# Kernel optimization log

Hardware: AMD Instinct MI355X
Metric: run time of the kernel (lower is better)

## Reference

```python
import jax, jax.numpy as jnp
import numpy as np

W0, W1 = 8, 8           # attn_grid_window_size
HEADS = 8
ATTN_CH = 256
HD = ATTN_CH // HEADS   # 32
LN_EPS = 1e-5
L2_EPS = 1e-12


def _rel_pos_index(h, w):
    # Swin-style relative position index, [h*w, h*w] int
    coords = np.stack(np.meshgrid(np.arange(h), np.arange(w), indexing='ij'))  # [2,h,w]
    coords = coords.reshape(2, -1)                                             # [2,L]
    rel = coords[:, :, None] - coords[:, None, :]                              # [2,L,L]
    rel = rel.transpose(1, 2, 0).astype(np.int64)                              # [L,L,2]
    rel[:, :, 0] += h - 1
    rel[:, :, 1] += w - 1
    rel[:, :, 0] *= 2 * w - 1
    return rel.sum(-1)                                                         # [L,L]

_REL_IDX = _rel_pos_index(W0, W1)


def _layernorm2d(x, g, b):
    # nn.LayerNorm((8,8)): normalize over the last two dims, affine shape (8,8)
    mu = jnp.mean(x, axis=(-2, -1), keepdims=True)
    var = jnp.var(x, axis=(-2, -1), keepdims=True)
    return (x - mu) * jax.lax.rsqrt(var + LN_EPS) * g + b


def setup_inputs() -> dict:
    key = jax.random.key(0)
    ks = jax.random.split(key, 8)
    C = 256
    return {
        'X': jax.random.normal(ks[0], (8, C, 128, 128), jnp.float32),
        'pre_gamma': jnp.ones((W0, W1), jnp.float32),
        'pre_beta': jnp.zeros((W0, W1), jnp.float32),
        'post_gamma': jnp.ones((W0, W1), jnp.float32),
        'post_beta': jnp.zeros((W0, W1), jnp.float32),
        'Wqkv': jax.random.normal(ks[1], (3 * ATTN_CH, C), jnp.float32) * 0.02,
        'bqkv': jnp.zeros((3 * ATTN_CH,), jnp.float32),
        'Wproj': jax.random.normal(ks[2], (C, ATTN_CH), jnp.float32) * 0.02,
        'bproj': jnp.zeros((C,), jnp.float32),
        'rel_bias_table': jax.random.normal(ks[3], ((2 * W0 - 1) * (2 * W1 - 1), HEADS), jnp.float32) * 0.02,
    }


def reference(X, pre_gamma, pre_beta, post_gamma, post_beta,
              Wqkv, bqkv, Wproj, bproj, rel_bias_table):
    N, C, H, W = X.shape
    L = W0 * W1
    # --- block partition (mirrors torch view/permute/contiguous().view) ---
    xp = X.reshape(N, C, H // W0, W0, W // W1, W1)
    xp = xp.transpose(0, 2, 4, 3, 5, 1).reshape(-1, C, W0, W1)  # [Bw, C, 8, 8]
    Bw = xp.shape[0]
    # --- pre-norm over the window dims ---
    xn = _layernorm2d(xp, pre_gamma, pre_beta)
    # --- windowed multi-head self-attention with relative position bias ---
    x = xn.reshape(Bw, C, L)
    qkv = jnp.einsum('oc,bcl->bol', Wqkv, x) + bqkv[None, :, None]   # [Bw, 3A, L]
    qkv = qkv.reshape(Bw, 3, HEADS, HD, L)
    q = qkv[:, 0].transpose(0, 1, 3, 2)  # [Bw, h, L, d]
    k = qkv[:, 1].transpose(0, 1, 3, 2)
    v = qkv[:, 2].transpose(0, 1, 3, 2)
    # MetNet-3 qk normalization (L2 normalize instead of 1/sqrt(d) scale)
    q = q / jnp.clip(jnp.linalg.norm(q, axis=-1, keepdims=True), L2_EPS)
    k = k / jnp.clip(jnp.linalg.norm(k, axis=-1, keepdims=True), L2_EPS)
    bias = rel_bias_table[jnp.asarray(_REL_IDX)].transpose(2, 0, 1)  # [h, L, L]
    attn = jnp.einsum('bhld,bhmd->bhlm', q, k) + bias[None]          # [Bw, h, L, L]
    attn = jax.nn.softmax(attn, axis=-1)
    out = jnp.einsum('bhlm,bhmd->bhld', attn, v)                     # [Bw, h, L, d]
    out = out.transpose(0, 1, 3, 2).reshape(Bw, ATTN_CH, L)          # [Bw, A, L]
    out = jnp.einsum('ca,bal->bcl', Wproj, out) + bproj[None, :, None]
    out = out.reshape(Bw, C, W0, W1)
    # --- residual, post-norm + Identity MLP residual ---
    y = xp + out
    y = y + _layernorm2d(y, post_gamma, post_beta)
    # --- reverse partition: composition of torch .view()s == plain reshape ---
    return y.reshape(N, C, H, W)
```

## Files before the change

### kernel.cpp

```cpp
#include <hip/hip_runtime.h>

typedef __bf16 bf16x8 __attribute__((ext_vector_type(8)));
typedef float  f32x4  __attribute__((ext_vector_type(4)));
typedef unsigned short ushort4v __attribute__((ext_vector_type(4)));

#define DEVI static __device__ __forceinline__

#define LDS_FENCE() do { \
  asm volatile("s_waitcnt lgkmcnt(0)" ::: "memory"); \
  __builtin_amdgcn_sched_barrier(0); \
} while (0)

DEVI unsigned short f2bf(float f) {
  __bf16 h = (__bf16)f;
  return __builtin_bit_cast(unsigned short, h);
}
DEVI float bf2f(unsigned short s) {
  union { unsigned u; float f; } v; v.u = ((unsigned)s) << 16;
  return v.f;
}

__global__ void prep_kernel(const float* __restrict__ Wqkv, const float* __restrict__ Wproj,
                            const float* __restrict__ table,
                            unsigned short* __restrict__ wq, unsigned short* __restrict__ wp,
                            float* __restrict__ biasg, float* __restrict__ rowsum) {
  const int i = blockIdx.x * 256 + threadIdx.x;
  if (i < 768 * 256) wq[i] = f2bf(Wqkv[i]);
  if (i < 256 * 256) wp[i] = f2bf(Wproj[i]);
  if (i < 8 * 64 * 64) {
    const int h = i >> 12, r = (i >> 6) & 63, c = i & 63;
    const int ridx = ((r >> 3) - (c >> 3) + 7) * 15 + ((r & 7) - (c & 7) + 7);
    biasg[i] = table[ridx * 8 + h];
  }
  if (i < 768) {
    const float4* p = reinterpret_cast<const float4*>(Wqkv + (size_t)i * 256);
    float s = 0.f;
#pragma unroll
    for (int j = 0; j < 64; ++j) { const float4 a = p[j]; s += a.x + a.y + a.z + a.w; }
    rowsum[i] = s;
  }
}

#define LDS_XN 0u
#define LDS_ST 32768u
#define LDS_Q  34816u
#define LDS_K  75776u
#define LDS_V  116736u
#define LDS_XW 34816u
#define LDS_YO 75776u
#define LDS_TOTAL 149504u

__global__ void __launch_bounds__(512, 2)
win_attn_kernel(const float* __restrict__ X,
                const float* __restrict__ preg, const float* __restrict__ preb,
                const float* __restrict__ postg, const float* __restrict__ postb,
                const float* __restrict__ bqkv, const float* __restrict__ bproj,
                const unsigned short* __restrict__ wq, const unsigned short* __restrict__ wp,
                const float* __restrict__ biasg, const float* __restrict__ rowsum,
                float* __restrict__ out) {
  __shared__ alignas(16) unsigned char sh[LDS_TOTAL];
  const int tid = threadIdx.x;
  const int w = tid >> 6;
  const int lane = tid & 63, lm = lane & 15, lg = lane >> 4;
  const int orig = blockIdx.x;
  const int b = (orig & 7) * 256 + (orig >> 3);
  const int n = b >> 8, gh = (b >> 4) & 15, gw = b & 15;
  const size_t wbase = (size_t)n * 4194304 + (size_t)gh * 1024 + (size_t)gw * 8;

  {
#pragma unroll
    for (int i = 0; i < 4; ++i) {
      const int rid = i * 512 + tid;
      const int cc = rid >> 3, w0 = rid & 7;
      const float* xb = X + wbase + (size_t)cc * 16384 + w0 * 128;
      const float4 a  = *reinterpret_cast<const float4*>(xb);
      const float4 bv = *reinterpret_cast<const float4*>(xb + 4);
      const unsigned xorv = (cc & 64) ? 16u : 0u;
      unsigned char* dst = sh + LDS_XW + (unsigned)cc * 272u + (unsigned)w0 * 32u;
      *reinterpret_cast<float4*>(dst + xorv)         = a;
      *reinterpret_cast<float4*>(dst + (16u ^ xorv)) = bv;
    }
  }
  __syncthreads();

  {
    const int c = tid >> 1, half = tid & 1;
    const int r = ((c >> 5) << 3) + ((c >> 2) & 7);
    const unsigned base = LDS_XW + (unsigned)(c & 3) * (64u * 272u)
                        + 4u * (unsigned)(r ^ ((c & 1) << 2));
    float fv[32];
    float s1 = 0.f, s2 = 0.f;
#pragma unroll
    for (int i = 0; i < 32; ++i) {
      const int l = half * 32 + i;
      const float v = *reinterpret_cast<const float*>(sh + base + (unsigned)l * 272u);
      fv[i] = v; s1 += v; s2 += v * v;
    }
    s1 += __shfl_xor(s1, 1);
    s2 += __shfl_xor(s2, 1);
    const float mean = s1 * (1.f / 64.f);
    float var = s2 * (1.f / 64.f) - mean * mean;
    var = fmaxf(var, 0.f) + 1e-5f;
    const float rstd = rsqrtf(var);
    const float sig  = var * rstd;
#pragma unroll
    for (int i = 0; i < 32; ++i) {
      const int l = half * 32 + i;
      *(unsigned short*)(sh + LDS_XN + l * 512 +
          (((unsigned)(2 * c)) ^ ((unsigned)((l & 7) << 4)))) = f2bf((fv[i] - mean) * rstd);
    }
    if (!half) *reinterpret_cast<float2*>(sh + LDS_ST + c * 8) = float2{mean, sig};
  }
  __syncthreads();

  {
    float pg4[4], pb4[4];
#pragma unroll
    for (int nt = 0; nt < 4; ++nt) { pg4[nt] = preg[nt * 16 + lm]; pb4[nt] = preb[nt * 16 + lm]; }
    const int wbase96 = w * 96;
    const unsigned char* abase = (const unsigned char*)wq + ((size_t)(wbase96 + lm) * 512 + lg * 16);
    f32x4 acc[6][4];
#pragma unroll
    for (int i = 0; i < 6; ++i)
#pragma unroll
      for (int j = 0; j < 4; ++j) acc[i][j] = f32x4{0.f, 0.f, 0.f, 0.f};
    bf16x8 acur[6];
#pragma unroll
    for (int m4 = 0; m4 < 6; ++m4)
      acur[m4] = *reinterpret_cast<const bf16x8*>(abase + m4 * 8192);
#pragma unroll
    for (int ks = 0; ks < 8; ++ks) {
      bf16x8 anxt[6];
      if (ks < 7) {
#pragma unroll
        for (int m4 = 0; m4 < 6; ++m4)
          anxt[m4] = *reinterpret_cast<const bf16x8*>(abase + m4 * 8192 + (ks + 1) * 64);
      }
      bf16x8 bfrag[4];
#pragma unroll
      for (int nt = 0; nt < 4; ++nt) {
        const int l = nt * 16 + lm;
        bfrag[nt] = *reinterpret_cast<const bf16x8*>(
            sh + LDS_XN + l * 512 + (((unsigned)(ks * 64 + lg * 16)) ^ ((unsigned)((l & 7) << 4))));
      }
#pragma unroll
      for (int m4 = 0; m4 < 6; ++m4)
#pragma unroll
        for (int nt = 0; nt < 4; ++nt)
          acc[m4][nt] = __builtin_amdgcn_mfma_f32_16x16x32_bf16(acur[m4], bfrag[nt], acc[m4][nt], 0, 0, 0);
      if (ks < 7) {
#pragma unroll
        for (int m4 = 0; m4 < 6; ++m4) acur[m4] = anxt[m4];
      }
    }
#pragma unroll
    for (int m4 = 0; m4 < 6; ++m4) {
      const f32x4 rs4 = *reinterpret_cast<const f32x4*>(rowsum + wbase96 + m4 * 16 + lg * 4);
      const f32x4 bq4 = *reinterpret_cast<const f32x4*>(bqkv   + wbase96 + m4 * 16 + lg * 4);
#pragma unroll
      for (int nt = 0; nt < 4; ++nt)
#pragma unroll
        for (int reg = 0; reg < 4; ++reg)
          acc[m4][nt][reg] = pg4[nt] * acc[m4][nt][reg] + pb4[nt] * rs4[reg] + bq4[reg];
    }
#pragma unroll
    for (int hh = 0; hh < 3; ++hh) {
      const int hh3 = w * 3 + hh;
      if (hh3 < 16) {
#pragma unroll
        for (int nt = 0; nt < 4; ++nt) {
          float ss = 0.f;
#pragma unroll
          for (int half = 0; half < 2; ++half)
#pragma unroll
            for (int reg = 0; reg < 4; ++reg) {
              const float v = acc[2 * hh + half][nt][reg];
              ss += v * v;
            }
          ss += __shfl_xor(ss, 16);
          ss += __shfl_xor(ss, 32);
          const float inv = 1.f / fmaxf(sqrtf(ss), 1e-12f);
#pragma unroll
          for (int half = 0; half < 2; ++half)
#pragma unroll
            for (int reg = 0; reg < 4; ++reg)
              acc[2 * hh + half][nt][reg] *= inv;
        }
      }
    }
#pragma unroll
    for (int hh = 0; hh < 3; ++hh) {
      const int hh3 = w * 3 + hh;
      if (hh3 < 16) {
        const unsigned base = (hh3 < 8) ? (LDS_Q + (unsigned)hh3 * 5120u)
                                        : (LDS_K + (unsigned)(hh3 - 8) * 5120u);
#pragma unroll
        for (int half = 0; half < 2; ++half) {
          const int d0 = half * 16 + lg * 4;
#pragma unroll
          for (int nt = 0; nt < 4; ++nt) {
            const int l = nt * 16 + lm;
            ushort4v pk;
#pragma unroll
            for (int reg = 0; reg < 4; ++reg) pk[reg] = f2bf(acc[2 * hh + half][nt][reg]);
            *reinterpret_cast<ushort4v*>(sh + base + l * 80 + 2 * d0) = pk;
          }
        }
      } else {
        const int hv = hh3 - 16;
#pragma unroll
        for (int half = 0; half < 2; ++half)
#pragma unroll
          for (int reg = 0; reg < 4; ++reg) {
            const int d = half * 16 + lg * 4 + reg;
#pragma unroll
            for (int nt = 0; nt < 4; ++nt) {
              const int l = nt * 16 + lm;
              *(unsigned short*)(sh + LDS_V + hv * 4096 + d * 128 +
                  (((unsigned)(2 * l)) ^ ((unsigned)((d & 7) << 4)))) =
                  f2bf(acc[2 * hh + half][nt][reg]);
            }
          }
      }
    }
  }
  __syncthreads();

  {
    const int h = w;
    const unsigned qh = LDS_Q + (unsigned)w * 5120u;
    const unsigned kh = LDS_K + (unsigned)w * 5120u;
    bf16x8 qf[4], kf[4], vf[2][2];
#pragma unroll
    for (int mt = 0; mt < 4; ++mt)
      qf[mt] = *reinterpret_cast<const bf16x8*>(sh + qh + (mt * 16 + lm) * 80 + lg * 16);
#pragma unroll
    for (int nt = 0; nt < 4; ++nt)
      kf[nt] = *reinterpret_cast<const bf16x8*>(sh + kh + (nt * 16 + lm) * 80 + lg * 16);
#pragma unroll
    for (int ks = 0; ks < 2; ++ks)
#pragma unroll
      for (int nt = 0; nt < 2; ++nt) {
        const int d = nt * 16 + lm;
        vf[ks][nt] = *reinterpret_cast<const bf16x8*>(
            sh + LDS_V + h * 4096 + d * 128 + (((unsigned)(ks * 64 + lg * 16)) ^ ((unsigned)((d & 7) << 4))));
      }
    LDS_FENCE();
    __syncthreads();

    const float* bh = biasg + h * 4096;
    float p[4][4][4];
#pragma unroll
    for (int mt = 0; mt < 4; ++mt)
#pragma unroll
      for (int reg = 0; reg < 4; ++reg) {
        const int rrow = mt * 16 + lg * 4 + reg;
#pragma unroll
        for (int nt = 0; nt < 4; ++nt)
          p[mt][nt][reg] = bh[rrow * 64 + nt * 16 + lm];
      }
    f32x4 s[4][4];
#pragma unroll
    for (int nt = 0; nt < 4; ++nt)
#pragma unroll
      for (int mt = 0; mt < 4; ++mt)
        s[mt][nt] = __builtin_amdgcn_mfma_f32_16x16x32_bf16(qf[mt], kf[nt], f32x4{0.f,0.f,0.f,0.f}, 0, 0, 0);
    float rinv[4][4];
#pragma unroll
    for (int mt = 0; mt < 4; ++mt)
#pragma unroll
      for (int reg = 0; reg < 4; ++reg) {
        float m = -1e30f;
#pragma unroll
        for (int nt = 0; nt < 4; ++nt) {
          const float v = s[mt][nt][reg] + p[mt][nt][reg];
          p[mt][nt][reg] = v;
          m = fmaxf(m, v);
        }
        m = fmaxf(m, __shfl_xor(m, 1));
        m = fmaxf(m, __shfl_xor(m, 2));
        m = fmaxf(m, __shfl_xor(m, 4));
        m = fmaxf(m, __shfl_xor(m, 8));
        float sum = 0.f;
#pragma unroll
        for (int nt = 0; nt < 4; ++nt) {
          const float e = __expf(p[mt][nt][reg] - m);
          p[mt][nt][reg] = e;
          sum += e;
        }
        sum += __shfl_xor(sum, 1);
        sum += __shfl_xor(sum, 2);
        sum += __shfl_xor(sum, 4);
        sum += __shfl_xor(sum, 8);
        rinv[mt][reg] = 1.f / sum;
      }
#pragma unroll
    for (int mt = 0; mt < 4; ++mt)
#pragma unroll
      for (int reg = 0; reg < 4; ++reg) {
        const int rrow = mt * 16 + lg * 4 + reg;
#pragma unroll
        for (int nt = 0; nt < 4; ++nt) {
          const int ccol = nt * 16 + lm;
          const unsigned flat = (unsigned)(rrow * 128) +
              (((unsigned)(2 * ccol)) ^ ((unsigned)((rrow & 7) << 4)));
          const unsigned addr = (flat < 5120u) ? (qh + flat) : (kh + flat - 5120u);
          *(unsigned short*)(sh + addr) = f2bf(p[mt][nt][reg] * rinv[mt][reg]);
        }
      }
    LDS_FENCE();
    f32x4 oacc[4][2];
#pragma unroll
    for (int mt = 0; mt < 4; ++mt) { oacc[mt][0] = f32x4{0.f,0.f,0.f,0.f}; oacc[mt][1] = f32x4{0.f,0.f,0.f,0.f}; }
#pragma unroll
    for (int ks = 0; ks < 2; ++ks) {
      bf16x8 pa[4];
#pragma unroll
      for (int mt = 0; mt < 4; ++mt) {
        const int l = mt * 16 + lm;
        const unsigned flat = (unsigned)(l * 128) +
            (((unsigned)(ks * 64 + lg * 16)) ^ ((unsigned)((l & 7) << 4)));
        const unsigned addr = (flat < 5120u) ? (qh + flat) : (kh + flat - 5120u);
        pa[mt] = *reinterpret_cast<const bf16x8*>(sh + addr);
      }
#pragma unroll
      for (int nt2 = 0; nt2 < 2; ++nt2)
#pragma unroll
        for (int mt = 0; mt < 4; ++mt)
          oacc[mt][nt2] = __builtin_amdgcn_mfma_f32_16x16x32_bf16(pa[mt], vf[ks][nt2], oacc[mt][nt2], 0, 0, 0);
    }
    LDS_FENCE();
#pragma unroll
    for (int mt = 0; mt < 4; ++mt)
#pragma unroll
      for (int reg = 0; reg < 4; ++reg) {
        const int l = mt * 16 + 4 * lg + reg;
#pragma unroll
        for (int nt2 = 0; nt2 < 2; ++nt2) {
          const int d = nt2 * 16 + lm;
          *(unsigned short*)(sh + qh + l * 80 + 2 * d) = f2bf(oacc[mt][nt2][reg]);
        }
      }
  }
  __syncthreads();

  {
    float pog4[4], pob4[4];
#pragma unroll
    for (int nt = 0; nt < 4; ++nt) { pog4[nt] = postg[nt * 16 + lm]; pob4[nt] = postb[nt * 16 + lm]; }
    const unsigned char* abase = (const unsigned char*)wp + ((size_t)(w * 32 + lm) * 512 + lg * 16);
    f32x4 acc[2][4];
#pragma unroll
    for (int i = 0; i < 2; ++i)
#pragma unroll
      for (int j = 0; j < 4; ++j) acc[i][j] = f32x4{0.f, 0.f, 0.f, 0.f};
    bf16x8 acur[2];
#pragma unroll
    for (int mt = 0; mt < 2; ++mt)
      acur[mt] = *reinterpret_cast<const bf16x8*>(abase + mt * 8192);
#pragma unroll
    for (int ks = 0; ks < 8; ++ks) {
      bf16x8 anxt[2];
      if (ks < 7) {
#pragma unroll
        for (int mt = 0; mt < 2; ++mt)
          anxt[mt] = *reinterpret_cast<const bf16x8*>(abase + mt * 8192 + (ks + 1) * 64);
      }
      bf16x8 bfr[4];
#pragma unroll
      for (int nt = 0; nt < 4; ++nt) {
        const int l = nt * 16 + lm;
        bfr[nt] = *reinterpret_cast<const bf16x8*>(sh + LDS_Q + (unsigned)ks * 5120 + l * 80 + lg * 16);
      }
#pragma unroll
      for (int mt = 0; mt < 2; ++mt)
#pragma unroll
        for (int nt = 0; nt < 4; ++nt)
          acc[mt][nt] = __builtin_amdgcn_mfma_f32_16x16x32_bf16(acur[mt], bfr[nt], acc[mt][nt], 0, 0, 0);
      if (ks < 7) {
#pragma unroll
        for (int mt = 0; mt < 2; ++mt) acur[mt] = anxt[mt];
      }
    }
#pragma unroll
    for (int mt = 0; mt < 2; ++mt) {
      const float4 bp4 = *reinterpret_cast<const float4*>(bproj + w * 32 + mt * 16 + lg * 4);
#pragma unroll
      for (int reg = 0; reg < 4; ++reg) {
        const int c = w * 32 + mt * 16 + lg * 4 + reg;
        const float bp = ((const float*)&bp4)[reg];
        const float2 ms = *reinterpret_cast<const float2*>(sh + LDS_ST + c * 8);
        float y[4];
        float s1 = 0.f, s2 = 0.f;
#pragma unroll
        for (int nt = 0; nt < 4; ++nt) {
          const int l = nt * 16 + lm;
          const float xh = bf2f(*(const unsigned short*)(
              sh + LDS_XN + l * 512 + (((unsigned)(2 * c)) ^ ((unsigned)((l & 7) << 4)))));
          const float v = xh * ms.y + ms.x + acc[mt][nt][reg] + bp;
          y[nt] = v;
          s1 += v; s2 += v * v;
        }
        s1 += __shfl_xor(s1, 1); s2 += __shfl_xor(s2, 1);
        s1 += __shfl_xor(s1, 2); s2 += __shfl_xor(s2, 2);
        s1 += __shfl_xor(s1, 4); s2 += __shfl_xor(s2, 4);
        s1 += __shfl_xor(s1, 8); s2 += __shfl_xor(s2, 8);
        const float mean = s1 * (1.f / 64.f);
        const float var  = s2 * (1.f / 64.f) - mean * mean;
        const float rstd = rsqrtf(fmaxf(var, 0.f) + 1e-5f);
#pragma unroll
        for (int nt = 0; nt < 4; ++nt) {
          const int l = nt * 16 + lm;
          const float v = y[nt];
          *reinterpret_cast<float*>(sh + LDS_YO + (unsigned)c * 256u +
              (((unsigned)(4 * l)) ^ ((unsigned)((c & 1) << 6)))) =
              v + (v - mean) * rstd * pog4[nt] + pob4[nt];
        }
      }
    }
  }
  __syncthreads();

  {
    const size_t ob = (size_t)b * 16384;
#pragma unroll
    for (int i = 0; i < 8; ++i) {
      const int flat = i * 512 + tid;
      const int c = flat >> 4, ch = flat & 15;
      const float4 v = *reinterpret_cast<const float4*>(
          sh + LDS_YO + (unsigned)c * 256u + (((unsigned)(ch * 16)) ^ ((unsigned)((c & 1) << 6))));
      *reinterpret_cast<float4*>(out + ob + (size_t)flat * 4) = v;
    }
  }
}

extern "C" void kernel_launch(void* const* d_in, const int* in_sizes, int n_in,
                              void* d_out, int out_size, void* d_ws, size_t ws_size,
                              hipStream_t stream) {
  const float* X     = (const float*)d_in[0];
  const float* preg  = (const float*)d_in[1];
  const float* preb  = (const float*)d_in[2];
  const float* postg = (const float*)d_in[3];
  const float* postb = (const float*)d_in[4];
  const float* Wqkv  = (const float*)d_in[5];
  const float* bqkv  = (const float*)d_in[6];
  const float* Wproj = (const float*)d_in[7];
  const float* bproj = (const float*)d_in[8];
  const float* table = (const float*)d_in[9];

  unsigned short* wq = (unsigned short*)d_ws;
  unsigned short* wp = (unsigned short*)((char*)d_ws + 393216);
  float* biasg       = (float*)((char*)d_ws + 524288);
  float* rowsum      = (float*)((char*)d_ws + 655360);

  prep_kernel<<<768, 256, 0, stream>>>(Wqkv, Wproj, table, wq, wp, biasg, rowsum);
  win_attn_kernel<<<2048, 512, 0, stream>>>(X, preg, preb, postg, postb,
                                            bqkv, bproj, wq, wp, biasg, rowsum,
                                            (float*)d_out);
}
```

Baseline: 292.3 us.

## Make each wave own one head end-to-end, keeping Q/K in registers

QKV projection rows are reassigned so each wave computes the Q, K and V rows of its own head. Q and K fragments then stay in registers and feed the score MFMA directly, computed transposed so softmax reductions run across lane groups. Only V and the attention output pass through a small per-wave LDS scratch, which cuts LDS use and drops several block-wide barriers. It also prefetches the weight fragments before barriers and writes the final output straight from registers with scalar stores instead of staging it through LDS, which risks less coalesced global writes.

Result: faster. 259.2 us (-11.3%).

```diff
diff --git a/kernel.cpp b/kernel.cpp
--- a/kernel.cpp
+++ b/kernel.cpp
@@ -2,7 +2,6 @@
 
 typedef __bf16 bf16x8 __attribute__((ext_vector_type(8)));
 typedef float  f32x4  __attribute__((ext_vector_type(4)));
-typedef unsigned short ushort4v __attribute__((ext_vector_type(4)));
 
 #define DEVI static __device__ __forceinline__
 
@@ -41,14 +40,11 @@
   }
 }
 
-#define LDS_XN 0u
-#define LDS_ST 32768u
-#define LDS_Q  34816u
-#define LDS_K  75776u
-#define LDS_V  116736u
-#define LDS_XW 34816u
-#define LDS_YO 75776u
-#define LDS_TOTAL 149504u
+#define LDS_XN  0u
+#define LDS_ST  32768u
+#define LDS_XW  34816u
+#define LDS_SCR 34816u
+#define LDS_TOTAL 104448u
 
 __global__ void __launch_bounds__(512, 2)
 win_attn_kernel(const float* __restrict__ X,
@@ -111,236 +107,190 @@
     }
     if (!half) *reinterpret_cast<float2*>(sh + LDS_ST + c * 8) = float2{mean, sig};
   }
+  const unsigned char* wqb = (const unsigned char*)wq;
+  size_t aoff[6];
+  bf16x8 acur[6];
+#pragma unroll
+  for (int t = 0; t < 6; ++t) {
+    const int o = (t >> 1) * 256 + 32 * w + 16 * (t & 1) + lm;
+    aoff[t] = (size_t)o * 512 + lg * 16;
+    acur[t] = *reinterpret_cast<const bf16x8*>(wqb + aoff[t]);
+  }
   __syncthreads();
 
-  {
-    float pg4[4], pb4[4];
-#pragma unroll
-    for (int nt = 0; nt < 4; ++nt) { pg4[nt] = preg[nt * 16 + lm]; pb4[nt] = preb[nt * 16 + lm]; }
-    const int wbase96 = w * 96;
-    const unsigned char* abase = (const unsigned char*)wq + ((size_t)(wbase96 + lm) * 512 + lg * 16);
-    f32x4 acc[6][4];
-#pragma unroll
-    for (int i = 0; i < 6; ++i)
-#pragma unroll
-      for (int j = 0; j < 4; ++j) acc[i][j] = f32x4{0.f, 0.f, 0.f, 0.f};
-    bf16x8 acur[6];
-#pragma unroll
-    for (int m4 = 0; m4 < 6; ++m4)
-      acur[m4] = *reinterpret_cast<const bf16x8*>(abase + m4 * 8192);
-#pragma unroll
-    for (int ks = 0; ks < 8; ++ks) {
-      bf16x8 anxt[6];
-      if (ks < 7) {
-#pragma unroll
-        for (int m4 = 0; m4 < 6; ++m4)
-          anxt[m4] = *reinterpret_cast<const bf16x8*>(abase + m4 * 8192 + (ks + 1) * 64);
-      }
-      bf16x8 bfrag[4];
+  float pg4[4], pb4[4];
+#pragma unroll
+  for (int nt = 0; nt < 4; ++nt) { pg4[nt] = preg[nt * 16 + lm]; pb4[nt] = preb[nt * 16 + lm]; }
+  f32x4 acc6[6][4];
+#pragma unroll
+  for (int t = 0; t < 6; ++t)
+#pragma unroll
+    for (int j = 0; j < 4; ++j) acc6[t][j] = f32x4{0.f, 0.f, 0.f, 0.f};
+#pragma unroll
+  for (int ks = 0; ks < 8; ++ks) {
+    bf16x8 anxt[6];
+    if (ks < 7) {
+#pragma unroll
+      for (int t = 0; t < 6; ++t)
+        anxt[t] = *reinterpret_cast<const bf16x8*>(wqb + aoff[t] + (ks + 1) * 64);
+    }
+    bf16x8 bfrag[4];
+#pragma unroll
+    for (int nt = 0; nt < 4; ++nt) {
+      const int l = nt * 16 + lm;
+      bfrag[nt] = *reinterpret_cast<const bf16x8*>(
+          sh + LDS_XN + l * 512 + (((unsigned)(ks * 64 + lg * 16)) ^ ((unsigned)((l & 7) << 4))));
+    }
+#pragma unroll
+    for (int t = 0; t < 6; ++t)
+#pragma unroll
+      for (int nt = 0; nt < 4; ++nt)
+        acc6[t][nt] = __builtin_amdgcn_mfma_f32_16x16x32_bf16(acur[t], bfrag[nt], acc6[t][nt], 0, 0, 0);
+    if (ks < 7) {
+#pragma unroll
+      for (int t = 0; t < 6; ++t) acur[t] = anxt[t];
+    }
+  }
+#pragma unroll
+  for (int t = 0; t < 6; ++t) {
+    const int ob = (t >> 1) * 256 + 32 * w + 16 * (t & 1);
+    const f32x4 rs4 = *reinterpret_cast<const f32x4*>(rowsum + ob + lg * 4);
+    const f32x4 bq4 = *reinterpret_cast<const f32x4*>(bqkv   + ob + lg * 4);
+#pragma unroll
+    for (int nt = 0; nt < 4; ++nt)
+#pragma unroll
+      for (int reg = 0; reg < 4; ++reg)
+        acc6[t][nt][reg] = pg4[nt] * acc6[t][nt][reg] + pb4[nt] * rs4[reg] + bq4[reg];
+  }
+#pragma unroll
+  for (int sec = 0; sec < 2; ++sec)
+#pragma unroll
+    for (int nt = 0; nt < 4; ++nt) {
+      float ss = 0.f;
+#pragma unroll
+      for (int sub = 0; sub < 2; ++sub)
+#pragma unroll
+        for (int reg = 0; reg < 4; ++reg) {
+          const float v = acc6[2 * sec + sub][nt][reg];
+          ss += v * v;
+        }
+      ss += __shfl_xor(ss, 16);
+      ss += __shfl_xor(ss, 32);
+      const float inv = 1.f / fmaxf(sqrtf(ss), 1e-12f);
+#pragma unroll
+      for (int sub = 0; sub < 2; ++sub)
+#pragma unroll
+        for (int reg = 0; reg < 4; ++reg)
+          acc6[2 * sec + sub][nt][reg] *= inv;
+    }
+
+  const unsigned scr = LDS_SCR + (unsigned)w * 4608u;
+  bf16x8 qfrag[4], kfrag[4];
+#pragma unroll
+  for (int nt = 0; nt < 4; ++nt) {
+    bf16x8 qv, kv;
+#pragma unroll
+    for (int sub = 0; sub < 2; ++sub)
+#pragma unroll
+      for (int reg = 0; reg < 4; ++reg) {
+        qv[sub * 4 + reg] = (__bf16)acc6[sub][nt][reg];
+        kv[sub * 4 + reg] = (__bf16)acc6[2 + sub][nt][reg];
+      }
+    qfrag[nt] = qv; kfrag[nt] = kv;
+  }
+#pragma unroll
+  for (int sub = 0; sub < 2; ++sub)
+#pragma unroll
+    for (int reg = 0; reg < 4; ++reg) {
+      const int d = 16 * sub + 4 * lg + reg;
 #pragma unroll
       for (int nt = 0; nt < 4; ++nt) {
-        const int l = nt * 16 + lm;
-        bfrag[nt] = *reinterpret_cast<const bf16x8*>(
-            sh + LDS_XN + l * 512 + (((unsigned)(ks * 64 + lg * 16)) ^ ((unsigned)((l & 7) << 4))));
-      }
-#pragma unroll
-      for (int m4 = 0; m4 < 6; ++m4)
-#pragma unroll
-        for (int nt = 0; nt < 4; ++nt)
-          acc[m4][nt] = __builtin_amdgcn_mfma_f32_16x16x32_bf16(acur[m4], bfrag[nt], acc[m4][nt], 0, 0, 0);
-      if (ks < 7) {
-#pragma unroll
-        for (int m4 = 0; m4 < 6; ++m4) acur[m4] = anxt[m4];
-      }
-    }
-#pragma unroll
-    for (int m4 = 0; m4 < 6; ++m4) {
-      const f32x4 rs4 = *reinterpret_cast<const f32x4*>(rowsum + wbase96 + m4 * 16 + lg * 4);
-      const f32x4 bq4 = *reinterpret_cast<const f32x4*>(bqkv   + wbase96 + m4 * 16 + lg * 4);
+        const int pcol = (nt >> 1) * 32 + (lm >> 2) * 8 + (nt & 1) * 4 + (lm & 3);
+        *(unsigned short*)(sh + scr + (unsigned)(d * 144 + 2 * pcol)) =
+            f2bf(acc6[4 + sub][nt][reg]);
+      }
+    }
+  LDS_FENCE();
+  bf16x8 vf[2][2];
+#pragma unroll
+  for (int ks = 0; ks < 2; ++ks)
+#pragma unroll
+    for (int mtd = 0; mtd < 2; ++mtd)
+      vf[ks][mtd] = *reinterpret_cast<const bf16x8*>(
+          sh + scr + (unsigned)((mtd * 16 + lm) * 144 + ks * 64 + lg * 16));
+  LDS_FENCE();
+
+  const float* bh = biasg + w * 4096;
+  f32x4 oaccT[2][4];
+#pragma unroll
+  for (int mtd = 0; mtd < 2; ++mtd)
+#pragma unroll
+    for (int nt = 0; nt < 4; ++nt) oaccT[mtd][nt] = f32x4{0.f, 0.f, 0.f, 0.f};
+#pragma unroll
+  for (int nt = 0; nt < 4; ++nt) {
+    f32x4 bb[4];
+#pragma unroll
+    for (int mt = 0; mt < 4; ++mt)
+      bb[mt] = *reinterpret_cast<const f32x4*>(bh + (nt * 16 + lm) * 64 + mt * 16 + 4 * lg);
+    f32x4 st[4];
+#pragma unroll
+    for (int mt = 0; mt < 4; ++mt)
+      st[mt] = __builtin_amdgcn_mfma_f32_16x16x32_bf16(kfrag[mt], qfrag[nt],
+                                                       f32x4{0.f,0.f,0.f,0.f}, 0, 0, 0);
+    float mmax = -1e30f;
+#pragma unroll
+    for (int mt = 0; mt < 4; ++mt)
+#pragma unroll
+      for (int reg = 0; reg < 4; ++reg) {
+        st[mt][reg] += bb[mt][reg];
+        mmax = fmaxf(mmax, st[mt][reg]);
+      }
+    mmax = fmaxf(mmax, __shfl_xor(mmax, 16));
+    mmax = fmaxf(mmax, __shfl_xor(mmax, 32));
+    float sum = 0.f;
+#pragma unroll
+    for (int mt = 0; mt < 4; ++mt)
+#pragma unroll
+      for (int reg = 0; reg < 4; ++reg) {
+        const float e = __expf(st[mt][reg] - mmax);
+        st[mt][reg] = e;
+        sum += e;
+      }
+    sum += __shfl_xor(sum, 16);
+    sum += __shfl_xor(sum, 32);
+    const float rinv = 1.f / sum;
+#pragma unroll
+    for (int ks = 0; ks < 2; ++ks) {
+      bf16x8 pf;
+#pragma unroll
+      for (int sub = 0; sub < 2; ++sub)
+#pragma unroll
+        for (int reg = 0; reg < 4; ++reg)
+          pf[sub * 4 + reg] = (__bf16)(st[2 * ks + sub][reg] * rinv);
+#pragma unroll
+      for (int mtd = 0; mtd < 2; ++mtd)
+        oaccT[mtd][nt] = __builtin_amdgcn_mfma_f32_16x16x32_bf16(vf[ks][mtd], pf,
+                                                                 oaccT[mtd][nt], 0, 0, 0);
+    }
+  }
+#pragma unroll
+  for (int mtd = 0; mtd < 2; ++mtd)
+#pragma unroll
+    for (int reg = 0; reg < 4; ++reg) {
+      const int d = mtd * 16 + 4 * lg + reg;
 #pragma unroll
       for (int nt = 0; nt < 4; ++nt)
-#pragma unroll
-        for (int reg = 0; reg < 4; ++reg)
-          acc[m4][nt][reg] = pg4[nt] * acc[m4][nt][reg] + pb4[nt] * rs4[reg] + bq4[reg];
-    }
-#pragma unroll
-    for (int hh = 0; hh < 3; ++hh) {
-      const int hh3 = w * 3 + hh;
-      if (hh3 < 16) {
-#pragma unroll
-        for (int nt = 0; nt < 4; ++nt) {
-          float ss = 0.f;
-#pragma unroll
-          for (int half = 0; half < 2; ++half)
-#pragma unroll
-            for (int reg = 0; reg < 4; ++reg) {
-              const float v = acc[2 * hh + half][nt][reg];
-              ss += v * v;
-            }
-          ss += __shfl_xor(ss, 16);
-          ss += __shfl_xor(ss, 32);
-          const float inv = 1.f / fmaxf(sqrtf(ss), 1e-12f);
-#pragma unroll
-          for (int half = 0; half < 2; ++half)
-#pragma unroll
-            for (int reg = 0; reg < 4; ++reg)
-              acc[2 * hh + half][nt][reg] *= inv;
-        }
-      }
-    }
-#pragma unroll
-    for (int hh = 0; hh < 3; ++hh) {
-      const int hh3 = w * 3 + hh;
-      if (hh3 < 16) {
-        const unsigned base = (hh3 < 8) ? (LDS_Q + (unsigned)hh3 * 5120u)
-                                        : (LDS_K + (unsigned)(hh3 - 8) * 5120u);
-#pragma unroll
-        for (int half = 0; half < 2; ++half) {
-          const int d0 = half * 16 + lg * 4;
-#pragma unroll
-          for (int nt = 0; nt < 4; ++nt) {
-            const int l = nt * 16 + lm;
-            ushort4v pk;
-#pragma unroll
-            for (int reg = 0; reg < 4; ++reg) pk[reg] = f2bf(acc[2 * hh + half][nt][reg]);
-            *reinterpret_cast<ushort4v*>(sh + base + l * 80 + 2 * d0) = pk;
-          }
-        }
-      } else {
-        const int hv = hh3 - 16;
-#pragma unroll
-        for (int half = 0; half < 2; ++half)
-#pragma unroll
-          for (int reg = 0; reg < 4; ++reg) {
-            const int d = half * 16 + lg * 4 + reg;
-#pragma unroll
-            for (int nt = 0; nt < 4; ++nt) {
-              const int l = nt * 16 + lm;
-              *(unsigned short*)(sh + LDS_V + hv * 4096 + d * 128 +
-                  (((unsigned)(2 * l)) ^ ((unsigned)((d & 7) << 4)))) =
-                  f2bf(acc[2 * hh + half][nt][reg]);
-            }
-          }
-      }
-    }
-  }
-  __syncthreads();
-
-  {
-    const int h = w;
-    const unsigned qh = LDS_Q + (unsigned)w * 5120u;
-    const unsigned kh = LDS_K + (unsigned)w * 5120u;
-    bf16x8 qf[4], kf[4], vf[2][2];
-#pragma unroll
-    for (int mt = 0; mt < 4; ++mt)
-      qf[mt] = *reinterpret_cast<const bf16x8*>(sh + qh + (mt * 16 + lm) * 80 + lg * 16);
-#pragma unroll
-    for (int nt = 0; nt < 4; ++nt)
-      kf[nt] = *reinterpret_cast<const bf16x8*>(sh + kh + (nt * 16 + lm) * 80 + lg * 16);
-#pragma unroll
-    for (int ks = 0; ks < 2; ++ks)
-#pragma unroll
-      for (int nt = 0; nt < 2; ++nt) {
-        const int d = nt * 16 + lm;
-        vf[ks][nt] = *reinterpret_cast<const bf16x8*>(
-            sh + LDS_V + h * 4096 + d * 128 + (((unsigned)(ks * 64 + lg * 16)) ^ ((unsigned)((d & 7) << 4))));
-      }
-    LDS_FENCE();
-    __syncthreads();
-
-    const float* bh = biasg + h * 4096;
-    float p[4][4][4];
-#pragma unroll
-    for (int mt = 0; mt < 4; ++mt)
-#pragma unroll
-      for (int reg = 0; reg < 4; ++reg) {
-        const int rrow = mt * 16 + lg * 4 + reg;
-#pragma unroll
-        for (int nt = 0; nt < 4; ++nt)
-          p[mt][nt][reg] = bh[rrow * 64 + nt * 16 + lm];
-      }
-    f32x4 s[4][4];
-#pragma unroll
-    for (int nt = 0; nt < 4; ++nt)
-#pragma unroll
-      for (int mt = 0; mt < 4; ++mt)
-        s[mt][nt] = __builtin_amdgcn_mfma_f32_16x16x32_bf16(qf[mt], kf[nt], f32x4{0.f,0.f,0.f,0.f}, 0, 0, 0);
-    float rinv[4][4];
-#pragma unroll
-    for (int mt = 0; mt < 4; ++mt)
-#pragma unroll
-      for (int reg = 0; reg < 4; ++reg) {
-        float m = -1e30f;
-#pragma unroll
-        for (int nt = 0; nt < 4; ++nt) {
-          const float v = s[mt][nt][reg] + p[mt][nt][reg];
-          p[mt][nt][reg] = v;
-          m = fmaxf(m, v);
-        }
-        m = fmaxf(m, __shfl_xor(m, 1));
-        m = fmaxf(m, __shfl_xor(m, 2));
-        m = fmaxf(m, __shfl_xor(m, 4));
-        m = fmaxf(m, __shfl_xor(m, 8));
-        float sum = 0.f;
-#pragma unroll
-        for (int nt = 0; nt < 4; ++nt) {
-          const float e = __expf(p[mt][nt][reg] - m);
-          p[mt][nt][reg] = e;
-          sum += e;
-        }
-        sum += __shfl_xor(sum, 1);
-        sum += __shfl_xor(sum, 2);
-        sum += __shfl_xor(sum, 4);
-        sum += __shfl_xor(sum, 8);
-        rinv[mt][reg] = 1.f / sum;
-      }
-#pragma unroll
-    for (int mt = 0; mt < 4; ++mt)
-#pragma unroll
-      for (int reg = 0; reg < 4; ++reg) {
-        const int rrow = mt * 16 + lg * 4 + reg;
-#pragma unroll
-        for (int nt = 0; nt < 4; ++nt) {
-          const int ccol = nt * 16 + lm;
-          const unsigned flat = (unsigned)(rrow * 128) +
-              (((unsigned)(2 * ccol)) ^ ((unsigned)((rrow & 7) << 4)));
-          const unsigned addr = (flat < 5120u) ? (qh + flat) : (kh + flat - 5120u);
-          *(unsigned short*)(sh + addr) = f2bf(p[mt][nt][reg] * rinv[mt][reg]);
-        }
-      }
-    LDS_FENCE();
-    f32x4 oacc[4][2];
-#pragma unroll
-    for (int mt = 0; mt < 4; ++mt) { oacc[mt][0] = f32x4{0.f,0.f,0.f,0.f}; oacc[mt][1] = f32x4{0.f,0.f,0.f,0.f}; }
-#pragma unroll
-    for (int ks = 0; ks < 2; ++ks) {
-      bf16x8 pa[4];
-#pragma unroll
-      for (int mt = 0; mt < 4; ++mt) {
-        const int l = mt * 16 + lm;
-        const unsigned flat = (unsigned)(l * 128) +
-            (((unsigned)(ks * 64 + lg * 16)) ^ ((unsigned)((l & 7) << 4)));
-        const unsigned addr = (flat < 5120u) ? (qh + flat) : (kh + flat - 5120u);
-        pa[mt] = *reinterpret_cast<const bf16x8*>(sh + addr);
-      }
-#pragma unroll
-      for (int nt2 = 0; nt2 < 2; ++nt2)
-#pragma unroll
-        for (int mt = 0; mt < 4; ++mt)
-          oacc[mt][nt2] = __builtin_amdgcn_mfma_f32_16x16x32_bf16(pa[mt], vf[ks][nt2], oacc[mt][nt2], 0, 0, 0);
-    }
-    LDS_FENCE();
-#pragma unroll
-    for (int mt = 0; mt < 4; ++mt)
-#pragma unroll
-      for (int reg = 0; reg < 4; ++reg) {
-        const int l = mt * 16 + 4 * lg + reg;
-#pragma unroll
-        for (int nt2 = 0; nt2 < 2; ++nt2) {
-          const int d = nt2 * 16 + lm;
-          *(unsigned short*)(sh + qh + l * 80 + 2 * d) = f2bf(oacc[mt][nt2][reg]);
-        }
-      }
+        *(unsigned short*)(sh + scr + (unsigned)((nt * 16 + lm) * 64 + 2 * d)) =
+            f2bf(oaccT[mtd][nt][reg]);
+    }
+
+  const unsigned char* wpb = (const unsigned char*)wp;
+  size_t poff[2];
+  bf16x8 pcur[2];
+#pragma unroll
+  for (int mt = 0; mt < 2; ++mt) {
+    poff[mt] = (size_t)(w * 32 + mt * 16 + lm) * 512 + lg * 16;
+    pcur[mt] = *reinterpret_cast<const bf16x8*>(wpb + poff[mt]);
   }
   __syncthreads();
 
@@ -348,38 +298,32 @@
     float pog4[4], pob4[4];
 #pragma unroll
     for (int nt = 0; nt < 4; ++nt) { pog4[nt] = postg[nt * 16 + lm]; pob4[nt] = postb[nt * 16 + lm]; }
-    const unsigned char* abase = (const unsigned char*)wp + ((size_t)(w * 32 + lm) * 512 + lg * 16);
-    f32x4 acc[2][4];
+    f32x4 pacc[2][4];
 #pragma unroll
     for (int i = 0; i < 2; ++i)
 #pragma unroll
-      for (int j = 0; j < 4; ++j) acc[i][j] = f32x4{0.f, 0.f, 0.f, 0.f};
-    bf16x8 acur[2];
-#pragma unroll
-    for (int mt = 0; mt < 2; ++mt)
-      acur[mt] = *reinterpret_cast<const bf16x8*>(abase + mt * 8192);
+      for (int j = 0; j < 4; ++j) pacc[i][j] = f32x4{0.f, 0.f, 0.f, 0.f};
 #pragma unroll
     for (int ks = 0; ks < 8; ++ks) {
-      bf16x8 anxt[2];
+      bf16x8 pnxt[2];
       if (ks < 7) {
 #pragma unroll
         for (int mt = 0; mt < 2; ++mt)
-          anxt[mt] = *reinterpret_cast<const bf16x8*>(abase + mt * 8192 + (ks + 1) * 64);
+          pnxt[mt] = *reinterpret_cast<const bf16x8*>(wpb + poff[mt] + (ks + 1) * 64);
       }
       bf16x8 bfr[4];
 #pragma unroll
-      for (int nt = 0; nt < 4; ++nt) {
-        const int l = nt * 16 + lm;
-        bfr[nt] = *reinterpret_cast<const bf16x8*>(sh + LDS_Q + (unsigned)ks * 5120 + l * 80 + lg * 16);
-      }
+      for (int nt = 0; nt < 4; ++nt)
+        bfr[nt] = *reinterpret_cast<const bf16x8*>(
+            sh + LDS_SCR + (unsigned)(ks * 4608 + (nt * 16 + lm) * 64 + lg * 16));
 #pragma unroll
       for (int mt = 0; mt < 2; ++mt)
 #pragma unroll
         for (int nt = 0; nt < 4; ++nt)
-          acc[mt][nt] = __builtin_amdgcn_mfma_f32_16x16x32_bf16(acur[mt], bfr[nt], acc[mt][nt], 0, 0, 0);
+          pacc[mt][nt] = __builtin_amdgcn_mfma_f32_16x16x32_bf16(pcur[mt], bfr[nt], pacc[mt][nt], 0, 0, 0);
       if (ks < 7) {
 #pragma unroll
-        for (int mt = 0; mt < 2; ++mt) acur[mt] = anxt[mt];
+        for (int mt = 0; mt < 2; ++mt) pcur[mt] = pnxt[mt];
       }
     }
 #pragma unroll
@@ -397,7 +341,7 @@
           const int l = nt * 16 + lm;
           const float xh = bf2f(*(const unsigned short*)(
               sh + LDS_XN + l * 512 + (((unsigned)(2 * c)) ^ ((unsigned)((l & 7) << 4)))));
-          const float v = xh * ms.y + ms.x + acc[mt][nt][reg] + bp;
+          const float v = xh * ms.y + ms.x + pacc[mt][nt][reg] + bp;
           y[nt] = v;
           s1 += v; s2 += v * v;
         }
@@ -408,28 +352,13 @@
         const float mean = s1 * (1.f / 64.f);
         const float var  = s2 * (1.f / 64.f) - mean * mean;
         const float rstd = rsqrtf(fmaxf(var, 0.f) + 1e-5f);
+        float* orow = out + (size_t)b * 16384 + (size_t)c * 64;
 #pragma unroll
         for (int nt = 0; nt < 4; ++nt) {
-          const int l = nt * 16 + lm;
           const float v = y[nt];
-          *reinterpret_cast<float*>(sh + LDS_YO + (unsigned)c * 256u +
-              (((unsigned)(4 * l)) ^ ((unsigned)((c & 1) << 6)))) =
-              v + (v - mean) * rstd * pog4[nt] + pob4[nt];
+          orow[nt * 16 + lm] = v + (v - mean) * rstd * pog4[nt] + pob4[nt];
         }
       }
-    }
-  }
-  __syncthreads();
-
-  {
-    const size_t ob = (size_t)b * 16384;
-#pragma unroll
-    for (int i = 0; i < 8; ++i) {
-      const int flat = i * 512 + tid;
-      const int c = flat >> 4, ch = flat & 15;
-      const float4 v = *reinterpret_cast<const float4*>(
-          sh + LDS_YO + (unsigned)c * 256u + (((unsigned)(ch * 16)) ^ ((unsigned)((c & 1) << 6))));
-      *reinterpret_cast<float4*>(out + ob + (size_t)flat * 4) = v;
     }
   }
 }
```
